# Performance work log

Measured on AMD Instinct MI355X. Metric: run time of the kernel, lower is better.

The kernel has to match this reference:

```python
import jax, jax.numpy as jnp
import numpy as np

B, T, INP, E, H, N = 16, 256, 1536, 512, 8, 16
D = E // H            # 64, must equal default dim_head for to_out shapes to work
SCALE = D ** -0.5
EPS = 1e-5


def _ln(x, g, b):
    m = x.mean(-1, keepdims=True)
    v = ((x - m) ** 2).mean(-1, keepdims=True)
    return (x - m) * jax.lax.rsqrt(v + EPS) * g + b


def _attend(q, k, v, Wo, bo):
    # q,k,v: [bt, h, n, d]. NOTE: attend is LogSoftmax, not Softmax (faithful).
    dots = jnp.einsum('bhnd,bhmd->bhnm', q, k) * SCALE
    a = jax.nn.log_softmax(dots, axis=-1)
    o = jnp.einsum('bhnm,bhmd->bhnd', a, v)
    o = o.transpose(0, 2, 1, 3).reshape(o.shape[0], N, E)  # b n (h d)
    return o @ Wo + bo


def _self_attn(x, Wqkv, Wo, bo):
    # x is already LayerNormed (PreNorm); residual adds the normed x (faithful).
    qkv = x @ Wqkv  # [bt, n, 3E]
    q, k, v = jnp.split(qkv, 3, axis=-1)
    hd = lambda t: t.reshape(t.shape[0], N, H, D).transpose(0, 2, 1, 3)
    return _attend(hd(q), hd(k), hd(v), Wo, bo) + x


def _ff(x, W1, b1, W2, b2):
    # x already LayerNormed; residual adds normed x (faithful to PreNorm+FF).
    return jax.nn.gelu(x @ W1 + b1, approximate=False) @ W2 + b2 + x


def setup_inputs() -> dict:
    key = jax.random.key(0)
    ks = iter(jax.random.split(key, 64))
    nrm = lambda shape, s=0.02: jax.random.normal(next(ks), shape, jnp.float32) * s
    inp = {
        'features': jax.random.normal(next(ks), (B, T, INP), jnp.float32),
        'targets_array': jax.random.randint(next(ks), (B, T), 0, N, jnp.int64),
        'emb': nrm((N, E), 1.0),
        'Wf': nrm((INP, 2 * E * N)), 'bf': jnp.zeros((2 * E * N,), jnp.float32),
        # layer 0: Attention (tuple path: only to_out used)
        'att0_Wo': nrm((E, E)), 'att0_bo': jnp.zeros((E,), jnp.float32),
        'Wm': nrm((E, 1)), 'bm': jnp.zeros((1,), jnp.float32),
    }
    for i in range(3):
        inp[f'ff{i}_g'] = jnp.ones((E,), jnp.float32)
        inp[f'ff{i}_b'] = jnp.zeros((E,), jnp.float32)
        inp[f'ff{i}_W1'] = nrm((E, 2 * E)); inp[f'ff{i}_b1'] = jnp.zeros((2 * E,), jnp.float32)
        inp[f'ff{i}_W2'] = nrm((2 * E, E)); inp[f'ff{i}_b2'] = jnp.zeros((E,), jnp.float32)
    for i in (1, 2):
        inp[f'att{i}_g'] = jnp.ones((E,), jnp.float32)
        inp[f'att{i}_b'] = jnp.zeros((E,), jnp.float32)
        inp[f'att{i}_Wqkv'] = nrm((E, 3 * E))
        inp[f'att{i}_Wo'] = nrm((E, E)); inp[f'att{i}_bo'] = jnp.zeros((E,), jnp.float32)
    return inp


def reference(features, targets_array, emb, Wf, bf, att0_Wo, att0_bo, Wm, bm,
              ff0_g, ff0_b, ff0_W1, ff0_b1, ff0_W2, ff0_b2,
              ff1_g, ff1_b, ff1_W1, ff1_b1, ff1_W2, ff1_b2,
              ff2_g, ff2_b, ff2_W1, ff2_b1, ff2_W2, ff2_b2,
              att1_g, att1_b, att1_Wqkv, att1_Wo, att1_bo,
              att2_g, att2_b, att2_Wqkv, att2_Wo, att2_bo):
    f = features.reshape(-1, INP)                 # [BT, INP]
    t = targets_array.reshape(-1)                 # [BT]
    kv = f @ Wf + bf                              # [BT, 2*E*N]
    k_, v_ = jnp.split(kv, 2, axis=-1)
    nhd = lambda x: x.reshape(-1, N, H, D).transpose(0, 2, 1, 3)  # b (n h d) -> b h n d
    k, v = nhd(k_), nhd(v_)
    q = emb[t].reshape(-1, H, 1, D)               # b h d -> b h 1 d
    q = jnp.broadcast_to(q, (q.shape[0], H, N, D))
    # layer stack: Attn(tuple), PreNorm(FF), PreNorm(Attn), PreNorm(FF), PreNorm(Attn), PreNorm(FF)
    x = _attend(q, k, v, att0_Wo, att0_bo)        # [BT, N, E]
    x = _ff(_ln(x, ff0_g, ff0_b), ff0_W1, ff0_b1, ff0_W2, ff0_b2)
    x = _self_attn(_ln(x, att1_g, att1_b), att1_Wqkv, att1_Wo, att1_bo)
    x = _ff(_ln(x, ff1_g, ff1_b), ff1_W1, ff1_b1, ff1_W2, ff1_b2)
    x = _self_attn(_ln(x, att2_g, att2_b), att2_Wqkv, att2_Wo, att2_bo)
    x = _ff(_ln(x, ff2_g, ff2_b), ff2_W1, ff2_b1, ff2_W2, ff2_b2)
    out = x.mean(axis=1)                          # mean over targets -> [BT, E]
    out = out.reshape(B, T, E)
    mean = out @ Wm + bm                          # [B, T, 1]
    return mean
```

## Files before the change

kernel.cpp:

```cpp
#include <hip/hip_runtime.h>
#include <math.h>

#define BTOT 4096
#define INP  1536
#define EDIM 512
#define NTOK 16
#define KVW  16384
#define ENW  8192
#define FFH  1024
#define NDOT 2048

typedef __attribute__((ext_vector_type(8))) __bf16 bf16x8;
typedef __attribute__((ext_vector_type(4))) float f32x4;

__device__ __forceinline__ ushort f2bf(float f) {
    union { float f; unsigned u; } v; v.f = f;
    unsigned r = v.u + 0x7fffu + ((v.u >> 16) & 1u);
    return (ushort)(r >> 16);
}
__device__ __forceinline__ float bf2f(ushort h) {
    union { unsigned u; float f; } v; v.u = ((unsigned)h) << 16;
    return v.f;
}

__device__ __forceinline__ void transpose_body(
    const float* in, int ld, int c0, int R, ushort* out,
    int bx, int by, int tid)
{
    __shared__ float t[64][65];
    const int bc = bx * 64 + c0;
    const int br = by * 64;
#pragma unroll
    for (int it = 0; it < 16; ++it) {
        int idx = tid + it * 256;
        int r = idx >> 6, c = idx & 63;
        t[r][c] = in[(size_t)(br + r) * ld + bc + c];
    }
    __syncthreads();
    const int C0 = bx * 64;
#pragma unroll
    for (int it = 0; it < 4; ++it) {
        int idx = tid + it * 256;
        int cc = idx >> 4, rp = idx & 15;
        uint2 w2;
        w2.x = f2bf(t[4 * rp + 0][cc]) | ((unsigned)f2bf(t[4 * rp + 1][cc]) << 16);
        w2.y = f2bf(t[4 * rp + 2][cc]) | ((unsigned)f2bf(t[4 * rp + 3][cc]) << 16);
        *reinterpret_cast<uint2*>(out + (size_t)(C0 + cc) * R + br + 4 * rp) = w2;
    }
}

struct TJob { const float* in; ushort* out; int ld, c0, R, gbx, boffs; };
struct TJobs { TJob j[10]; };

__global__ __launch_bounds__(256) void transpose_all_k(TJobs jobs)
{
    const int b = blockIdx.x;
    int ji = 0;
    while (ji < 9 && b >= jobs.j[ji + 1].boffs) ++ji;
    TJob jb = jobs.j[ji];
    const int rel = b - jb.boffs;
    transpose_body(jb.in, jb.ld, jb.c0, jb.R, jb.out,
                   rel % jb.gbx, rel / jb.gbx, threadIdx.x);
}

__global__ __launch_bounds__(256) void conv_all_k(
    const float* __restrict__ features, ushort* __restrict__ featb,
    const float* __restrict__ wq0, const float* __restrict__ wq1,
    ushort* __restrict__ wv0, ushort* __restrict__ wv1)
{
    const int b = blockIdx.x;
    if (b < 3072) {
        const int i = b * 256 + threadIdx.x;
        const float4* p = reinterpret_cast<const float4*>(features) + 2 * (size_t)i;
        float4 a = p[0], c = p[1];
        uint4 o;
        o.x = f2bf(a.x) | ((unsigned)f2bf(a.y) << 16);
        o.y = f2bf(a.z) | ((unsigned)f2bf(a.w) << 16);
        o.z = f2bf(c.x) | ((unsigned)f2bf(c.y) << 16);
        o.w = f2bf(c.z) | ((unsigned)f2bf(c.w) << 16);
        reinterpret_cast<uint4*>(featb)[i] = o;
    } else {
        const int bb = b - 3072;
        const float* src = (bb >= 128) ? wq1 : wq0;
        ushort* dst = (bb >= 128) ? wv1 : wv0;
        const int idx = (bb & 127) * 256 + threadIdx.x;
        const int row = idx >> 6, c8 = (idx & 63) * 8;
        const float4* p = reinterpret_cast<const float4*>(
            src + (size_t)row * (3 * EDIM) + 2 * EDIM + c8);
        float4 a = p[0], c = p[1];
        uint4 o;
        o.x = f2bf(a.x) | ((unsigned)f2bf(a.y) << 16);
        o.y = f2bf(a.z) | ((unsigned)f2bf(a.w) << 16);
        o.z = f2bf(c.x) | ((unsigned)f2bf(c.y) << 16);
        o.w = f2bf(c.z) | ((unsigned)f2bf(c.w) << 16);
        *reinterpret_cast<uint4*>(dst + (size_t)row * EDIM + c8) = o;
    }
}

__global__ __launch_bounds__(256) void gproj_k(
    const float* __restrict__ Wf, const float* __restrict__ bfv,
    const float* __restrict__ emb, ushort* __restrict__ BTg,
    float* __restrict__ C0s, const int* __restrict__ targets,
    int* __restrict__ perm, int* __restrict__ boff)
{
    if (blockIdx.y == 8) {
        if (blockIdx.x != 0) return;
        __shared__ int cnt[NTOK], off_s[NTOK], cur[NTOK];
        const int tid = threadIdx.x;
        if (tid < NTOK) cnt[tid] = 0;
        __syncthreads();
        for (int i = tid; i < BTOT; i += 256) atomicAdd(&cnt[targets[i]], 1);
        __syncthreads();
        if (tid == 0) {
            int s = 0;
            for (int b = 0; b < NTOK; ++b) { off_s[b] = s; cur[b] = s; s += cnt[b]; }
            for (int b = 0; b < NTOK; ++b) boff[b] = off_s[b];
            boff[NTOK] = s;
        }
        __syncthreads();
        for (int i = tid; i < BTOT; i += 256) {
            int t = targets[i];
            int p = atomicAdd(&cur[t], 1);
            perm[p] = i;
        }
        return;
    }

    const int hm = blockIdx.x;
    const int h = hm >> 4, m = hm & 15;
    const int l = threadIdx.x & 63, w = threadIdx.x >> 6;
    const int t = l & 15, isub = l >> 4;
    const int colb = m * 512 + h * 64;
    const int ibase = blockIdx.y * (INP / 8);

    float4 e[16];
#pragma unroll
    for (int q = 0; q < 16; ++q)
        e[q] = *reinterpret_cast<const float4*>(emb + t * EDIM + h * 64 + q * 4);

    const int n = t * 128 + hm;
    for (int i0 = ibase; i0 < ibase + INP / 8; i0 += 16) {
        const int i = i0 + w * 4 + isub;
        const float* wr = Wf + (size_t)i * KVW + colb;
        float acc = 0.f;
#pragma unroll
        for (int q = 0; q < 16; ++q) {
            float4 v4 = *reinterpret_cast<const float4*>(wr + q * 4);
            acc = fmaf(v4.x, e[q].x, fmaf(v4.y, e[q].y,
                  fmaf(v4.z, e[q].z, fmaf(v4.w, e[q].w, acc))));
        }
        BTg[(size_t)n * INP + i] = f2bf(acc);
    }
    if (blockIdx.y == 0 && w == 0 && isub == 0) {
        const float* br = bfv + colb;
        float acc = 0.f;
#pragma unroll
        for (int q = 0; q < 16; ++q) {
            float4 v4 = *reinterpret_cast<const float4*>(br + q * 4);
            acc = fmaf(v4.x, e[q].x, fmaf(v4.y, e[q].y,
                  fmaf(v4.z, e[q].z, fmaf(v4.w, e[q].w, acc))));
        }
        C0s[n] = 0.125f * acc;
    }
}

template <int BM, int BN, int WM, int WN, int NW, bool GELU, bool OUTBF>
__global__ __launch_bounds__(NW * 64) void gemm_mfma_k(
    const ushort* __restrict__ A, int lda,
    const ushort* __restrict__ BT, int ldb,
    void* __restrict__ Cp, int ldc, int K,
    const float* __restrict__ bias,
    const float* __restrict__ res, int ldr,
    float scale)
{
    static_assert((BM / WM) * (BN / WN) == NW, "wave grid");
    static_assert(BM % (NW * 8) == 0 && BN % (NW * 8) == 0, "staging");
    constexpr int FM = WM / 16, FN = WN / 16;
    constexpr int IA = BM * 8 / (NW * 64), IB = BN * 8 / (NW * 64);
    constexpr int RA = BM / NW, RB = BN / NW;

    __shared__ bf16x8 As[BM][8];
    __shared__ bf16x8 Bs[BN][8];
    const int tid = threadIdx.x;
    const int l   = tid & 63;
    const int w   = tid >> 6;
    const int wm  = w / (BN / WN), wn = w % (BN / WN);
    const int brow = blockIdx.y * BM, bcol = blockIdx.x * BN;

    const int lr = l >> 3;
    const int ls = (l & 7) ^ lr;
    const ushort* Ab = A  + (size_t)(brow + w * RA + lr) * lda + ls * 8;
    const ushort* Bb = BT + (size_t)(bcol + w * RB + lr) * ldb + ls * 8;

    f32x4 acc[FM][FN];
#pragma unroll
    for (int i = 0; i < FM; ++i)
#pragma unroll
        for (int j = 0; j < FN; ++j) acc[i][j] = (f32x4)0.f;

    for (int k0 = 0; k0 < K; k0 += 64) {
#pragma unroll
        for (int i = 0; i < IA; ++i)
            __builtin_amdgcn_global_load_lds(
                (const __attribute__((address_space(1))) void*)(Ab + (size_t)(i * 8) * lda + k0),
                (__attribute__((address_space(3))) void*)&As[w * RA + i * 8][0],
                16, 0, 0);
#pragma unroll
        for (int i = 0; i < IB; ++i)
            __builtin_amdgcn_global_load_lds(
                (const __attribute__((address_space(1))) void*)(Bb + (size_t)(i * 8) * ldb + k0),
                (__attribute__((address_space(3))) void*)&Bs[w * RB + i * 8][0],
                16, 0, 0);
        __syncthreads();
#pragma unroll
        for (int kh = 0; kh < 2; ++kh) {
            const int slot = (kh * 4 + (l >> 4)) ^ (l & 7);
            bf16x8 af[FM], bfr[FN];
#pragma unroll
            for (int mt = 0; mt < FM; ++mt)
                af[mt] = As[wm * WM + mt * 16 + (l & 15)][slot];
#pragma unroll
            for (int nt = 0; nt < FN; ++nt)
                bfr[nt] = Bs[wn * WN + nt * 16 + (l & 15)][slot];
#pragma unroll
            for (int mt = 0; mt < FM; ++mt)
#pragma unroll
                for (int nt = 0; nt < FN; ++nt)
                    acc[mt][nt] = __builtin_amdgcn_mfma_f32_16x16x32_bf16(
                        af[mt], bfr[nt], acc[mt][nt], 0, 0, 0);
        }
        __syncthreads();
    }

    const int cr = (l >> 4) * 4, cc = l & 15;
#pragma unroll
    for (int mt = 0; mt < FM; ++mt) {
#pragma unroll
        for (int nt = 0; nt < FN; ++nt) {
            const int gc = bcol + wn * WN + nt * 16 + cc;
            const float bv = bias ? bias[gc] : 0.f;
#pragma unroll
            for (int r = 0; r < 4; ++r) {
                const size_t gr = (size_t)brow + wm * WM + mt * 16 + cr + r;
                float v = acc[mt][nt][r] * scale + bv;
                if (GELU) v = 0.5f * v * (1.f + erff(v * 0.70710678118654752f));
                if (res) v += res[gr * ldr + gc];
                if (OUTBF) ((ushort*)Cp)[gr * ldc + gc] = f2bf(v);
                else       ((float*)Cp)[gr * ldc + gc]  = v;
            }
        }
    }
}

__global__ __launch_bounds__(512, 2) void gemm_v256_k(
    const ushort* __restrict__ A,
    const ushort* __restrict__ BT,
    const float* __restrict__ bias,
    ushort* __restrict__ C)
{
    __shared__ bf16x8 lds[2][2][256][8];
    const int tid = threadIdx.x;
    const int l = tid & 63, w = tid >> 6;
    const int wm = w >> 2, wn = w & 3;
    const int brow = blockIdx.y * 256, bcol = blockIdx.x * 256;
    const int lr = l >> 3, ls = (l & 7) ^ lr;

    const ushort* Ab = A  + (size_t)(brow + w * 8 + lr) * INP + ls * 8;
    const ushort* Bb = BT + (size_t)(bcol + w * 8 + lr) * INP + ls * 8;

#define STAGE_T(d, t) do { const int k0s = (t) * 64;                          \
    _Pragma("unroll")                                                          \
    for (int g = 0; g < 4; ++g)                                                \
        __builtin_amdgcn_global_load_lds(                                      \
            (const __attribute__((address_space(1))) void*)(Ab + (size_t)(g * 64) * INP + k0s), \
            (__attribute__((address_space(3))) void*)&lds[d][0][g * 64 + w * 8][0], 16, 0, 0);  \
    _Pragma("unroll")                                                          \
    for (int g = 0; g < 4; ++g)                                                \
        __builtin_amdgcn_global_load_lds(                                      \
            (const __attribute__((address_space(1))) void*)(Bb + (size_t)(g * 64) * INP + k0s), \
            (__attribute__((address_space(3))) void*)&lds[d][1][g * 64 + w * 8][0], 16, 0, 0);  \
} while (0)

    f32x4 acc[8][4];
#pragma unroll
    for (int i = 0; i < 8; ++i)
#pragma unroll
        for (int j = 0; j < 4; ++j) acc[i][j] = (f32x4)0.f;

    STAGE_T(0, 0);
    STAGE_T(1, 1);
    asm volatile("s_waitcnt vmcnt(8)" ::: "memory");
    __builtin_amdgcn_s_barrier();

    const int NT = INP / 64;
    for (int j = 0; j < NT; ++j) {
        const int d = j & 1;
        const bool st = (j > 0 && j < NT - 1);
        const int k0s = (j + 1) * 64;
        bf16x8 bfr[4][2];
#pragma unroll
        for (int p = 0; p < 4; ++p) {
            const int rh = p >> 1, kh = p & 1;
            const int slot = (kh * 4 + (l >> 4)) ^ (l & 7);
            bf16x8 a[4];
#pragma unroll
            for (int mt = 0; mt < 4; ++mt)
                a[mt] = lds[d][0][wm * 128 + rh * 64 + mt * 16 + (l & 15)][slot];
            if (p < 2) {
#pragma unroll
                for (int nt = 0; nt < 4; ++nt)
                    bfr[nt][kh] = lds[d][1][wn * 64 + nt * 16 + (l & 15)][slot];
            }
            if (st) {
#pragma unroll
                for (int q = 0; q < 2; ++q) {
                    const int idx = 2 * p + q;
                    if (idx < 4)
                        __builtin_amdgcn_global_load_lds(
                            (const __attribute__((address_space(1))) void*)(
                                Ab + (size_t)(idx * 64) * INP + k0s),
                            (__attribute__((address_space(3))) void*)
                                &lds[d ^ 1][0][idx * 64 + w * 8][0], 16, 0, 0);
                    else
                        __builtin_amdgcn_global_load_lds(
                            (const __attribute__((address_space(1))) void*)(
                                Bb + (size_t)((idx - 4) * 64) * INP + k0s),
                            (__attribute__((address_space(3))) void*)
                                &lds[d ^ 1][1][(idx - 4) * 64 + w * 8][0], 16, 0, 0);
                }
            }
            __builtin_amdgcn_s_barrier();
            asm volatile("s_waitcnt lgkmcnt(0)" ::: "memory");
            __builtin_amdgcn_sched_barrier(0);
            __builtin_amdgcn_s_setprio(1);
#pragma unroll
            for (int mt = 0; mt < 4; ++mt)
#pragma unroll
                for (int nt = 0; nt < 4; ++nt)
                    acc[rh * 4 + mt][nt] = __builtin_amdgcn_mfma_f32_16x16x32_bf16(
                        a[mt], bfr[nt][kh], acc[rh * 4 + mt][nt], 0, 0, 0);
            __builtin_amdgcn_s_setprio(0);
            if (p == 3) asm volatile("s_waitcnt vmcnt(0)" ::: "memory");
            __builtin_amdgcn_s_barrier();
        }
    }
#undef STAGE_T

    const int cr = (l >> 4) * 4, cc = l & 15;
#pragma unroll
    for (int h = 0; h < 2; ++h)
#pragma unroll
        for (int mt = 0; mt < 4; ++mt)
#pragma unroll
            for (int nt = 0; nt < 4; ++nt) {
                const int gc = bcol + wn * 64 + nt * 16 + cc;
                const float bv = bias[gc];
#pragma unroll
                for (int r = 0; r < 4; ++r) {
                    const size_t gr = (size_t)brow + wm * 128 + h * 64 + mt * 16 + cr + r;
                    C[gr * ENW + gc] = f2bf(acc[h * 4 + mt][nt][r] + bv);
                }
            }
}

__global__ __launch_bounds__(256) void gemm_dots_k(
    const ushort* __restrict__ A,
    const ushort* __restrict__ BT,
    const int* __restrict__ perm, const int* __restrict__ boff,
    const float* __restrict__ C0s, float* __restrict__ Csel)
{
    const int bucket = blockIdx.y;
    const int off = boff[bucket], end = boff[bucket + 1];
    const int tile = blockIdx.x;
    if (tile * 128 >= end - off) return;

    __shared__ bf16x8 As[128][8];
    __shared__ bf16x8 Bs[128][8];
    const int tid = threadIdx.x;
    const int l = tid & 63, w = tid >> 6;
    const int wm = w >> 1, wn = w & 1;
    const int lr = l >> 3;
    const int ls = (l & 7) ^ lr;

    int rowidx[4];
#pragma unroll
    for (int i = 0; i < 4; ++i) {
        int rg = off + tile * 128 + w * 32 + lr + i * 8;
        rowidx[i] = perm[rg < end ? rg : off];
    }
    const ushort* Bb = BT + (size_t)(bucket * 128 + w * 32 + lr) * INP + ls * 8;

    f32x4 acc[4][4];
#pragma unroll
    for (int i = 0; i < 4; ++i)
#pragma unroll
        for (int j = 0; j < 4; ++j) acc[i][j] = (f32x4)0.f;

    for (int k0 = 0; k0 < INP; k0 += 64) {
#pragma unroll
        for (int i = 0; i < 4; ++i)
            __builtin_amdgcn_global_load_lds(
                (const __attribute__((address_space(1))) void*)(
                    A + (size_t)rowidx[i] * INP + ls * 8 + k0),
                (__attribute__((address_space(3))) void*)&As[w * 32 + i * 8][0],
                16, 0, 0);
#pragma unroll
        for (int i = 0; i < 4; ++i)
            __builtin_amdgcn_global_load_lds(
                (const __attribute__((address_space(1))) void*)(
                    Bb + (size_t)(i * 8) * INP + k0),
                (__attribute__((address_space(3))) void*)&Bs[w * 32 + i * 8][0],
                16, 0, 0);
        __syncthreads();
#pragma unroll
        for (int kh = 0; kh < 2; ++kh) {
            const int slot = (kh * 4 + (l >> 4)) ^ (l & 7);
            bf16x8 af[4], bfr[4];
#pragma unroll
            for (int mt = 0; mt < 4; ++mt)
                af[mt] = As[wm * 64 + mt * 16 + (l & 15)][slot];
#pragma unroll
            for (int nt = 0; nt < 4; ++nt)
                bfr[nt] = Bs[wn * 64 + nt * 16 + (l & 15)][slot];
#pragma unroll
            for (int mt = 0; mt < 4; ++mt)
#pragma unroll
                for (int nt = 0; nt < 4; ++nt)
                    acc[mt][nt] = __builtin_amdgcn_mfma_f32_16x16x32_bf16(
                        af[mt], bfr[nt], acc[mt][nt], 0, 0, 0);
        }
        __syncthreads();
    }

    const int cr = (l >> 4) * 4, cc = l & 15;
#pragma unroll
    for (int mt = 0; mt < 4; ++mt) {
#pragma unroll
        for (int nt = 0; nt < 4; ++nt) {
            const int gc = wn * 64 + nt * 16 + cc;
            const float bv = C0s[bucket * 128 + gc];
#pragma unroll
            for (int r = 0; r < 4; ++r) {
                float val = acc[mt][nt][r] * 0.125f + bv;
                float mx = val;
                mx = fmaxf(mx, __shfl_xor(mx, 1, 64));
                mx = fmaxf(mx, __shfl_xor(mx, 2, 64));
                mx = fmaxf(mx, __shfl_xor(mx, 4, 64));
                mx = fmaxf(mx, __shfl_xor(mx, 8, 64));
                float e = expf(val - mx);
                e += __shfl_xor(e, 1, 64);
                e += __shfl_xor(e, 2, 64);
                e += __shfl_xor(e, 4, 64);
                e += __shfl_xor(e, 8, 64);
                const float lse = mx + logf(e);
                int rg = off + tile * 128 + wm * 64 + mt * 16 + cr + r;
                int orow = perm[rg < end ? rg : off];
                Csel[(size_t)orow * 128 + gc] = val - lse;
            }
        }
    }
}

__global__ __launch_bounds__(512) void attend0_k(
    const float* __restrict__ dsel, const ushort* __restrict__ vb,
    ushort* __restrict__ o)
{
    const int bt = blockIdx.x;
    const int l  = threadIdx.x & 63;
    const int h  = threadIdx.x >> 6;
    const int dg = l & 7, mg = l >> 3;

    const float w0 = dsel[(size_t)bt * 128 + h * 16 + mg];
    const float w1 = dsel[(size_t)bt * 128 + h * 16 + 8 + mg];

    const ushort* base = vb + (size_t)bt * ENW + h * 64 + dg * 8;
    uint4 v0 = *reinterpret_cast<const uint4*>(base + (size_t)mg * EDIM);
    uint4 v1 = *reinterpret_cast<const uint4*>(base + (size_t)(8 + mg) * EDIM);
    const ushort* u0 = reinterpret_cast<const ushort*>(&v0);
    const ushort* u1 = reinterpret_cast<const ushort*>(&v1);
    float acc[8];
#pragma unroll
    for (int j = 0; j < 8; ++j)
        acc[j] = w0 * bf2f(u0[j]) + w1 * bf2f(u1[j]);
#pragma unroll
    for (int off = 8; off < 64; off <<= 1)
#pragma unroll
        for (int j = 0; j < 8; ++j) acc[j] += __shfl_xor(acc[j], off, 64);

    if (mg == 0) {
        uint4 pk;
        pk.x = f2bf(acc[0]) | ((unsigned)f2bf(acc[1]) << 16);
        pk.y = f2bf(acc[2]) | ((unsigned)f2bf(acc[3]) << 16);
        pk.z = f2bf(acc[4]) | ((unsigned)f2bf(acc[5]) << 16);
        pk.w = f2bf(acc[6]) | ((unsigned)f2bf(acc[7]) << 16);
        *reinterpret_cast<uint4*>(o + (size_t)bt * EDIM + h * 64 + dg * 8) = pk;
    }
}

__global__ __launch_bounds__(256) void ln_k(
    const float* __restrict__ x, const float* __restrict__ g,
    const float* __restrict__ b, float* __restrict__ y,
    ushort* __restrict__ yb)
{
    const int row = blockIdx.x * 4 + (threadIdx.x >> 6);
    const int lane = threadIdx.x & 63;
    const float* xr = x + (size_t)row * EDIM + lane * 8;
    float4 a0 = *reinterpret_cast<const float4*>(xr);
    float4 a1 = *reinterpret_cast<const float4*>(xr + 4);
    float v[8] = {a0.x, a0.y, a0.z, a0.w, a1.x, a1.y, a1.z, a1.w};

    float s = 0.f;
#pragma unroll
    for (int j = 0; j < 8; ++j) s += v[j];
#pragma unroll
    for (int off = 32; off; off >>= 1) s += __shfl_xor(s, off, 64);
    const float m = s * (1.f / 512.f);

    float q = 0.f;
#pragma unroll
    for (int j = 0; j < 8; ++j) { float d = v[j] - m; q = fmaf(d, d, q); }
#pragma unroll
    for (int off = 32; off; off >>= 1) q += __shfl_xor(q, off, 64);
    const float inv = rsqrtf(q * (1.f / 512.f) + 1e-5f);

    const int c = lane * 8;
    float4 g0 = *reinterpret_cast<const float4*>(g + c);
    float4 g1 = *reinterpret_cast<const float4*>(g + c + 4);
    float4 b0 = *reinterpret_cast<const float4*>(b + c);
    float4 b1 = *reinterpret_cast<const float4*>(b + c + 4);
    float gg[8] = {g0.x, g0.y, g0.z, g0.w, g1.x, g1.y, g1.z, g1.w};
    float bb[8] = {b0.x, b0.y, b0.z, b0.w, b1.x, b1.y, b1.z, b1.w};
    float out[8];
#pragma unroll
    for (int j = 0; j < 8; ++j) out[j] = (v[j] - m) * inv * gg[j] + bb[j];
    float* yr = y + (size_t)row * EDIM + c;
    *reinterpret_cast<float4*>(yr) = make_float4(out[0], out[1], out[2], out[3]);
    *reinterpret_cast<float4*>(yr + 4) = make_float4(out[4], out[5], out[6], out[7]);
    uint4 p;
    p.x = f2bf(out[0]) | ((unsigned)f2bf(out[1]) << 16);
    p.y = f2bf(out[2]) | ((unsigned)f2bf(out[3]) << 16);
    p.z = f2bf(out[4]) | ((unsigned)f2bf(out[5]) << 16);
    p.w = f2bf(out[6]) | ((unsigned)f2bf(out[7]) << 16);
    *reinterpret_cast<uint4*>(yb + (size_t)row * EDIM + c) = p;
}

__global__ __launch_bounds__(256) void final_k(
    const float* __restrict__ x, const float* __restrict__ Wm,
    const float* __restrict__ bm, float* __restrict__ out)
{
    const int row = blockIdx.x * 4 + (threadIdx.x >> 6);
    const int lane = threadIdx.x & 63;
    const float* xr = x + (size_t)row * EDIM + lane * 8;
    const float* wr = Wm + lane * 8;
    float s = 0.f;
#pragma unroll
    for (int j = 0; j < 8; ++j) s = fmaf(xr[j], wr[j], s);
#pragma unroll
    for (int off = 32; off; off >>= 1) s += __shfl_xor(s, off, 64);
    if (lane == 0) out[row] = s + bm[0];
}

extern "C" void kernel_launch(void* const* d_in, const int* in_sizes, int n_in,
                              void* d_out, int out_size, void* d_ws, size_t ws_size,
                              hipStream_t stream)
{
    (void)in_sizes; (void)n_in; (void)out_size; (void)ws_size;
    const float* features = (const float*)d_in[0];
    const int*   targets  = (const int*)d_in[1];
    const float* emb      = (const float*)d_in[2];
    const float* Wf       = (const float*)d_in[3];
    const float* bfv      = (const float*)d_in[4];
    const float* a0Wo     = (const float*)d_in[5];
    const float* a0bo     = (const float*)d_in[6];
    const float* Wm       = (const float*)d_in[7];
    const float* bm       = (const float*)d_in[8];
    const float *ffg[3], *ffb[3], *W1[3], *b1[3], *W2[3], *b2[3];
    for (int i = 0; i < 3; ++i) {
        ffg[i] = (const float*)d_in[9 + 6 * i];
        ffb[i] = (const float*)d_in[10 + 6 * i];
        W1[i]  = (const float*)d_in[11 + 6 * i];
        b1[i]  = (const float*)d_in[12 + 6 * i];
        W2[i]  = (const float*)d_in[13 + 6 * i];
        b2[i]  = (const float*)d_in[14 + 6 * i];
    }
    const float *ag[2], *abp[2], *aWqkv[2], *aWo[2], *abo[2];
    for (int i = 0; i < 2; ++i) {
        ag[i]    = (const float*)d_in[27 + 5 * i];
        abp[i]   = (const float*)d_in[28 + 5 * i];
        aWqkv[i] = (const float*)d_in[29 + 5 * i];
        aWo[i]   = (const float*)d_in[30 + 5 * i];
        abo[i]   = (const float*)d_in[31 + 5 * i];
    }

    char* wsc = (char*)d_ws;
    auto alloc = [&](size_t bytes) { char* p = wsc; wsc += bytes; return p; };
    ushort* WfvT  = (ushort*)alloc((size_t)ENW * INP * 2);
    ushort* BTg   = (ushort*)alloc((size_t)NDOT * INP * 2);
    float*  C0s   = (float*) alloc((size_t)NDOT * 4);
    float*  dsel  = (float*) alloc((size_t)BTOT * 128 * 4);
    int*    perm  = (int*)   alloc((size_t)BTOT * 4);
    int*    boff  = (int*)   alloc(32 * 4);
    ushort* a0WoT = (ushort*)alloc((size_t)EDIM * EDIM * 2);
    ushort *W1T[3], *W2T[3], *WoT[2], *Wv_bf[2], *WcombT[2];
    for (int i = 0; i < 3; ++i) {
        W1T[i] = (ushort*)alloc((size_t)FFH * EDIM * 2);
        W2T[i] = (ushort*)alloc((size_t)EDIM * FFH * 2);
    }
    for (int i = 0; i < 2; ++i) {
        WoT[i]    = (ushort*)alloc((size_t)EDIM * EDIM * 2);
        Wv_bf[i]  = (ushort*)alloc((size_t)EDIM * EDIM * 2);
        WcombT[i] = (ushort*)alloc((size_t)EDIM * EDIM * 2);
    }
    ushort* featb = (ushort*)alloc((size_t)BTOT * INP * 2);
    ushort* o_b   = (ushort*)alloc((size_t)BTOT * EDIM * 2);
    float*  x     = (float*) alloc((size_t)BTOT * EDIM * 4);
    float*  xln   = (float*) alloc((size_t)BTOT * EDIM * 4);
    ushort* xlnb  = (ushort*)alloc((size_t)BTOT * EDIM * 2);
    ushort* hb    = (ushort*)alloc((size_t)BTOT * FFH * 2);
    ushort* vb    = (ushort*)alloc((size_t)BTOT * ENW * 2);

    const dim3 blk(256, 1, 1);

    conv_all_k<<<3328, blk, 0, stream>>>(features, featb,
                                         aWqkv[0], aWqkv[1], Wv_bf[0], Wv_bf[1]);
    gproj_k<<<dim3(128, 9), blk, 0, stream>>>(Wf, bfv, emb, BTg, C0s,
                                              targets, perm, boff);

    TJobs tj;
    int ob = 0, ji = 0;
    auto addj = [&](const float* in, ushort* out, int ld, int c0, int R,
                    int gbx, int gby) {
        tj.j[ji++] = {in, out, ld, c0, R, gbx, ob};
        ob += gbx * gby;
    };
    addj(Wf, WfvT, KVW, ENW, INP, 128, 24);
    addj(a0Wo, a0WoT, EDIM, 0, EDIM, 8, 8);
    for (int i = 0; i < 3; ++i) {
        addj(W1[i], W1T[i], FFH, 0, EDIM, 16, 8);
        addj(W2[i], W2T[i], EDIM, 0, FFH, 8, 16);
    }
    addj(aWo[0], WoT[0], EDIM, 0, EDIM, 8, 8);
    addj(aWo[1], WoT[1], EDIM, 0, EDIM, 8, 8);
    transpose_all_k<<<ob, blk, 0, stream>>>(tj);

    const float CATT = -44.36141955583650f;
    gemm_dots_k<<<dim3(32, 16), blk, 0, stream>>>(featb, BTg, perm, boff,
                                                  C0s, dsel);
    for (int i = 0; i < 2; ++i)
        gemm_mfma_k<64, 128, 32, 64, 4, false, true>
            <<<dim3(EDIM / 128, EDIM / 64), blk, 0, stream>>>(
            WoT[i], EDIM, Wv_bf[i], EDIM, WcombT[i], EDIM, EDIM,
            nullptr, nullptr, 0, CATT);
    gemm_v256_k<<<dim3(ENW / 256, BTOT / 256), dim3(512, 1, 1), 0, stream>>>(
        featb, WfvT, bfv + ENW, vb);
    attend0_k<<<BTOT, 512, 0, stream>>>(dsel, vb, o_b);
    gemm_mfma_k<64, 128, 32, 64, 4, false, false>
        <<<dim3(EDIM / 128, BTOT / 64), blk, 0, stream>>>(
        o_b, EDIM, a0WoT, EDIM, x, EDIM, EDIM, a0bo, nullptr, 0, 1.f);

    auto ln = [&](const float* g, const float* b) {
        ln_k<<<BTOT / 4, blk, 0, stream>>>(x, g, b, xln, xlnb);
    };
    auto ff = [&](int i) {
        ln(ffg[i], ffb[i]);
        gemm_mfma_k<64, 128, 32, 64, 4, true, true>
            <<<dim3(FFH / 128, BTOT / 64), blk, 0, stream>>>(
            xlnb, EDIM, W1T[i], EDIM, hb, FFH, EDIM, b1[i], nullptr, 0, 1.f);
        gemm_mfma_k<64, 128, 32, 64, 4, false, false>
            <<<dim3(EDIM / 128, BTOT / 64), blk, 0, stream>>>(
            hb, FFH, W2T[i], FFH, x, EDIM, FFH, b2[i], xln, EDIM, 1.f);
    };
    auto attn = [&](int i) {
        ln(ag[i], abp[i]);
        gemm_mfma_k<64, 128, 32, 64, 4, false, false>
            <<<dim3(EDIM / 128, BTOT / 64), blk, 0, stream>>>(
            xlnb, EDIM, WcombT[i], EDIM, x, EDIM, EDIM, abo[i], xln, EDIM, 1.f);
    };

    ff(0);
    attn(0);
    ff(1);
    attn(1);
    ff(2);

    final_k<<<BTOT / 4, blk, 0, stream>>>(x, Wm, bm, (float*)d_out);
}
```

Baseline: 474.0 us.

## Restructure big V GEMM loop with register prefetch, XCD-aware block mapping, larger FF1 tiles

```diff
diff --git a/kernel.cpp b/kernel.cpp
--- a/kernel.cpp
+++ b/kernel.cpp
@@ -262,7 +262,11 @@
     const int tid = threadIdx.x;
     const int l = tid & 63, w = tid >> 6;
     const int wm = w >> 2, wn = w & 3;
-    const int brow = blockIdx.y * 256, bcol = blockIdx.x * 256;
+    const int b = blockIdx.x;
+    const int xcd = b & 7, bi = b >> 3;
+    const int bx = xcd * 4 + (bi >> 4);
+    const int by = bi & 15;
+    const int brow = by * 256, bcol = bx * 256;
     const int lr = l >> 3, ls = (l & 7) ^ lr;
 
     const ushort* Ab = A  + (size_t)(brow + w * 8 + lr) * INP + ls * 8;
@@ -281,6 +285,31 @@
             (__attribute__((address_space(3))) void*)&lds[d][1][g * 64 + w * 8][0], 16, 0, 0);  \
 } while (0)
 
+#define RD_A(dst, dd, rh, kh) do {                                             \
+    const int slot_ = ((kh) * 4 + (l >> 4)) ^ (l & 7);                         \
+    _Pragma("unroll")                                                          \
+    for (int mt = 0; mt < 4; ++mt)                                             \
+        dst[mt] = lds[dd][0][wm * 128 + (rh) * 64 + mt * 16 + (l & 15)][slot_]; \
+} while (0)
+
+#define RD_B(dd, kh) do {                                                      \
+    const int slot_ = ((kh) * 4 + (l >> 4)) ^ (l & 7);                         \
+    _Pragma("unroll")                                                          \
+    for (int nt = 0; nt < 4; ++nt)                                             \
+        bfr[nt][kh] = lds[dd][1][wn * 64 + nt * 16 + (l & 15)][slot_];         \
+} while (0)
+
+#define MFMA4(base, af, kh) do {                                               \
+    __builtin_amdgcn_s_setprio(1);                                             \
+    _Pragma("unroll")                                                          \
+    for (int mt = 0; mt < 4; ++mt)                                             \
+        _Pragma("unroll")                                                      \
+        for (int nt = 0; nt < 4; ++nt)                                         \
+            acc[(base) + mt][nt] = __builtin_amdgcn_mfma_f32_16x16x32_bf16(    \
+                af[mt], bfr[nt][kh], acc[(base) + mt][nt], 0, 0, 0);           \
+    __builtin_amdgcn_s_setprio(0);                                             \
+} while (0)
+
     f32x4 acc[8][4];
 #pragma unroll
     for (int i = 0; i < 8; ++i)
@@ -292,59 +321,32 @@
     asm volatile("s_waitcnt vmcnt(8)" ::: "memory");
     __builtin_amdgcn_s_barrier();
 
+    bf16x8 aA[4], aB[4], bfr[4][2];
+    RD_A(aA, 0, 0, 0);
+    RD_B(0, 0);
+
     const int NT = INP / 64;
     for (int j = 0; j < NT; ++j) {
         const int d = j & 1;
-        const bool st = (j > 0 && j < NT - 1);
-        const int k0s = (j + 1) * 64;
-        bf16x8 bfr[4][2];
-#pragma unroll
-        for (int p = 0; p < 4; ++p) {
-            const int rh = p >> 1, kh = p & 1;
-            const int slot = (kh * 4 + (l >> 4)) ^ (l & 7);
-            bf16x8 a[4];
-#pragma unroll
-            for (int mt = 0; mt < 4; ++mt)
-                a[mt] = lds[d][0][wm * 128 + rh * 64 + mt * 16 + (l & 15)][slot];
-            if (p < 2) {
-#pragma unroll
-                for (int nt = 0; nt < 4; ++nt)
-                    bfr[nt][kh] = lds[d][1][wn * 64 + nt * 16 + (l & 15)][slot];
-            }
-            if (st) {
-#pragma unroll
-                for (int q = 0; q < 2; ++q) {
-                    const int idx = 2 * p + q;
-                    if (idx < 4)
-                        __builtin_amdgcn_global_load_lds(
-                            (const __attribute__((address_space(1))) void*)(
-                                Ab + (size_t)(idx * 64) * INP + k0s),
-                            (__attribute__((address_space(3))) void*)
-                                &lds[d ^ 1][0][idx * 64 + w * 8][0], 16, 0, 0);
-                    else
-                        __builtin_amdgcn_global_load_lds(
-                            (const __attribute__((address_space(1))) void*)(
-                                Bb + (size_t)((idx - 4) * 64) * INP + k0s),
-                            (__attribute__((address_space(3))) void*)
-                                &lds[d ^ 1][1][(idx - 4) * 64 + w * 8][0], 16, 0, 0);
-                }
-            }
-            __builtin_amdgcn_s_barrier();
-            asm volatile("s_waitcnt lgkmcnt(0)" ::: "memory");
-            __builtin_amdgcn_sched_barrier(0);
-            __builtin_amdgcn_s_setprio(1);
-#pragma unroll
-            for (int mt = 0; mt < 4; ++mt)
-#pragma unroll
-                for (int nt = 0; nt < 4; ++nt)
-                    acc[rh * 4 + mt][nt] = __builtin_amdgcn_mfma_f32_16x16x32_bf16(
-                        a[mt], bfr[nt][kh], acc[rh * 4 + mt][nt], 0, 0, 0);
-            __builtin_amdgcn_s_setprio(0);
-            if (p == 3) asm volatile("s_waitcnt vmcnt(0)" ::: "memory");
-            __builtin_amdgcn_s_barrier();
+        if (j > 0 && j + 1 < NT) STAGE_T(d ^ 1, j + 1);
+        RD_A(aB, d, 0, 1);
+        RD_B(d, 1);
+        MFMA4(0, aA, 0);
+        RD_A(aA, d, 1, 0);
+        MFMA4(0, aB, 1);
+        RD_A(aB, d, 1, 1);
+        MFMA4(4, aA, 0);
+        MFMA4(4, aB, 1);
+        __syncthreads();
+        if (j + 1 < NT) {
+            RD_A(aA, d ^ 1, 0, 0);
+            RD_B(d ^ 1, 0);
         }
     }
 #undef STAGE_T
+#undef RD_A
+#undef RD_B
+#undef MFMA4
 
     const int cr = (l >> 4) * 4, cc = l & 15;
 #pragma unroll
@@ -651,7 +653,7 @@
             <<<dim3(EDIM / 128, EDIM / 64), blk, 0, stream>>>(
             WoT[i], EDIM, Wv_bf[i], EDIM, WcombT[i], EDIM, EDIM,
             nullptr, nullptr, 0, CATT);
-    gemm_v256_k<<<dim3(ENW / 256, BTOT / 256), dim3(512, 1, 1), 0, stream>>>(
+    gemm_v256_k<<<512, dim3(512, 1, 1), 0, stream>>>(
         featb, WfvT, bfv + ENW, vb);
     attend0_k<<<BTOT, 512, 0, stream>>>(dsel, vb, o_b);
     gemm_mfma_k<64, 128, 32, 64, 4, false, false>
@@ -663,8 +665,8 @@
     };
     auto ff = [&](int i) {
         ln(ffg[i], ffb[i]);
-        gemm_mfma_k<64, 128, 32, 64, 4, true, true>
-            <<<dim3(FFH / 128, BTOT / 64), blk, 0, stream>>>(
+        gemm_mfma_k<128, 128, 64, 64, 4, true, true>
+            <<<dim3(FFH / 128, BTOT / 128), blk, 0, stream>>>(
             xlnb, EDIM, W1T[i], EDIM, hb, FFH, EDIM, b1[i], nullptr, 0, 1.f);
         gemm_mfma_k<64, 128, 32, 64, 4, false, false>
             <<<dim3(EDIM / 128, BTOT / 64), blk, 0, stream>>>(
```

After: 563.8 us. +19.0%, slower.
